# Optimization experiments

Measured on AMD Instinct MI355X. Metric: run time of the kernel, lower is better.

## Reference

```python
import jax, jax.numpy as jnp
import numpy as np

NUM_EXPERTS = 8
TOP_K = 2
CAPACITY_FACTOR = 1.25
D_MODEL = 2048
HIDDEN = 2048
N_TOKENS = 4096


def _expert_capacity(n_tokens):
    ideal = TOP_K * n_tokens / NUM_EXPERTS
    allowed = int(CAPACITY_FACTOR * ideal)
    return ((allowed + 7) // 8) * 8  # ensure_multiple_of(..., 8)


def setup_inputs() -> dict:
    key = jax.random.key(0)
    ks = jax.random.split(key, 6)
    x = jax.random.normal(ks[0], (N_TOKENS, D_MODEL), dtype=jnp.float32)
    ew = jax.random.uniform(ks[1], (N_TOKENS, TOP_K), dtype=jnp.float32)
    expert_weights = ew / jnp.sum(ew, axis=-1, keepdims=True)  # router softmax-like weights
    expert_indices = jax.random.randint(ks[2], (N_TOKENS, TOP_K), 0, NUM_EXPERTS, dtype=jnp.int32)
    s = 1.0 / np.sqrt(D_MODEL)
    w1 = jax.random.normal(ks[3], (NUM_EXPERTS, D_MODEL, HIDDEN), dtype=jnp.float32) * s
    w3 = jax.random.normal(ks[4], (NUM_EXPERTS, D_MODEL, HIDDEN), dtype=jnp.float32) * s
    w2 = jax.random.normal(ks[5], (NUM_EXPERTS, HIDDEN, D_MODEL), dtype=jnp.float32) * (1.0 / np.sqrt(HIDDEN))
    return {"x": x, "expert_weights": expert_weights, "expert_indices": expert_indices,
            "w1": w1, "w2": w2, "w3": w3}


def reference(x, expert_weights, expert_indices, w1, w2, w3):
    N, d = x.shape
    E = NUM_EXPERTS
    cap = _expert_capacity(N)
    T = N * TOP_K

    flat_e = expert_indices.reshape(-1)                      # [T]
    # histc: tokens per expert
    counts = jnp.zeros((E,), jnp.int32).at[flat_e].add(1)
    # stable sort by expert id (torch.sort on ints is stable here semantically)
    order = jnp.argsort(flat_e, stable=True)                 # [T]
    sorted_e = flat_e[order]
    starts = jnp.cumsum(counts) - counts                     # bin start offsets
    pos = jnp.arange(T, dtype=jnp.int32) - starts[sorted_e]  # rank within expert bin
    valid = pos < cap                                        # drop tokens over capacity
    tok = order // TOP_K                                     # source token per routed slot

    # binned_gather -> [E, cap, d]
    dest = jnp.where(valid, sorted_e * cap + pos, 0)
    xg = jnp.zeros((E * cap, d), x.dtype).at[dest].add(
        jnp.where(valid[:, None], x[tok], 0.0))
    xg = xg.reshape(E, cap, d)

    # grouped SwiGLU MLP per expert
    h = jax.nn.silu(jnp.einsum('ecd,edh->ech', xg, w1)) * jnp.einsum('ecd,edh->ech', xg, w3)
    ye = jnp.einsum('ech,ehd->ecd', h, w2).reshape(E * cap, d)

    # binned_scatter with expert weights (combine)
    w_flat = expert_weights.reshape(-1)[order]               # [T]
    contrib = ye[dest] * (w_flat * valid.astype(x.dtype))[:, None]
    y = jnp.zeros((N, d), x.dtype).at[tok].add(contrib)
    return y, counts
```

## Files before the change

### kernel.cpp

```cpp
#include <hip/hip_runtime.h>
#include <cstdint>

#define NEXP 8
#define TOPK 2
#define NTOK 4096
#define NSLOT (NTOK * TOPK)
#define CAP 1280
#define DM 2048
#define EC (NEXP * CAP)

typedef __bf16 bf16x8 __attribute__((ext_vector_type(8)));
typedef float  f32x4  __attribute__((ext_vector_type(4)));
typedef int    i32x4  __attribute__((ext_vector_type(4)));
typedef int    i32x8  __attribute__((ext_vector_type(8)));

typedef const void __attribute__((address_space(1))) gvoid;
typedef void __attribute__((address_space(3))) lvoid;

__device__ __forceinline__ void gld16(const void* g, void* l) {
  __builtin_amdgcn_global_load_lds((gvoid*)(uintptr_t)g, (lvoid*)(uintptr_t)l,
                                   16, 0, 0);
}

__device__ __forceinline__ unsigned fp8x4(float a, float b, float c, float d) {
  int v = __builtin_amdgcn_cvt_pk_fp8_f32(a, b, 0, false);
  v = __builtin_amdgcn_cvt_pk_fp8_f32(c, d, v, true);
  return (unsigned)v;
}
__device__ __forceinline__ unsigned char fp8one(float a) {
  return (unsigned char)(__builtin_amdgcn_cvt_pk_fp8_f32(a, a, 0, false) & 0xff);
}

__global__ void route_k(const int* __restrict__ eidx, int* __restrict__ row_token,
                        int* __restrict__ slot_dest, int* __restrict__ mcount,
                        float* __restrict__ out) {
  __shared__ int lh[256][NEXP];
  int tid = threadIdx.x;
  for (int i = tid; i < EC; i += 256) row_token[i] = -1;
#pragma unroll
  for (int e = 0; e < NEXP; ++e) lh[tid][e] = 0;
  __syncthreads();
  int base = tid * 32;
  for (int j = 0; j < 32; ++j) lh[tid][eidx[base + j]]++;
  __syncthreads();
  if (tid < NEXP) {
    int run = 0;
    for (int i = 0; i < 256; ++i) { int t = lh[i][tid]; lh[i][tid] = run; run += t; }
    mcount[tid] = run < CAP ? run : CAP;
    out[(size_t)NTOK * DM + tid] = (float)run;
  }
  __syncthreads();
  for (int j = 0; j < 32; ++j) {
    int t = base + j;
    int e = eidx[t];
    int r = lh[tid][e]++;
    if (r < CAP) { int dst = e * CAP + r; slot_dest[t] = dst; row_token[dst] = t >> 1; }
    else slot_dest[t] = -1;
  }
}

__device__ __forceinline__ void transT_tile(const float* __restrict__ w,
                                            unsigned char* __restrict__ wT,
                                            int e, int n0, int k0, char* smem) {
  float (*t)[69] = (float (*)[69])smem;
  const float* src = w + ((size_t)e << 22) + (size_t)k0 * DM + n0;
  unsigned char* dst = wT + ((size_t)e << 22) + (size_t)n0 * DM + k0;
  int c4 = (threadIdx.x & 15) * 4, r0 = threadIdx.x >> 4;
#pragma unroll
  for (int p = 0; p < 4; ++p) {
    int r = p * 16 + r0;
    float4 v = *(const float4*)(src + (size_t)r * DM + c4);
    t[r][c4 + 0] = v.x; t[r][c4 + 1] = v.y; t[r][c4 + 2] = v.z; t[r][c4 + 3] = v.w;
  }
  __syncthreads();
  int j = threadIdx.x & 7, rr0 = threadIdx.x >> 3;
#pragma unroll
  for (int q = 0; q < 2; ++q) {
    int rr = q * 32 + rr0;
    int k8 = j * 8;
    uint2 v;
    v.x = fp8x4(t[k8 + 0][rr], t[k8 + 1][rr], t[k8 + 2][rr], t[k8 + 3][rr]);
    v.y = fp8x4(t[k8 + 4][rr], t[k8 + 5][rr], t[k8 + 6][rr], t[k8 + 7][rr]);
    *(uint2*)(dst + (size_t)rr * DM + k8) = v;
  }
}

__global__ __launch_bounds__(256)
void prep_k(const float* __restrict__ w1, const float* __restrict__ w3,
            unsigned char* __restrict__ wT1, unsigned char* __restrict__ wT3,
            const float* __restrict__ x, const int* __restrict__ row_token,
            unsigned char* __restrict__ xg) {
  __shared__ __align__(16) char smem[64 * 69 * 4];
  int bid = blockIdx.x;
  if (bid < 16384) {
    const float* w = (bid & 8192) ? w3 : w1;
    unsigned char* wT = (bid & 8192) ? wT3 : wT1;
    int rem = bid & 8191;
    int e = rem >> 10, t = rem & 1023;
    transT_tile(w, wT, e, (t & 31) * 64, (t >> 5) * 64, smem);
  } else {
    int rbase = (bid - 16384) * 8;
    int c = threadIdx.x * 8;
#pragma unroll 1
    for (int i = 0; i < 8; ++i) {
      int r = rbase + i;
      int tok = row_token[r];
      uint2 o;
      if (tok >= 0) {
        const float* src = x + (size_t)tok * DM + c;
        float4 a = *(const float4*)src;
        float4 b = *(const float4*)(src + 4);
        o.x = fp8x4(a.x, a.y, a.z, a.w);
        o.y = fp8x4(b.x, b.y, b.z, b.w);
      } else { o.x = 0u; o.y = 0u; }
      *(uint2*)(xg + (size_t)r * DM + c) = o;
    }
  }
}

__global__ __launch_bounds__(256, 2)
void gemm13t_k(const unsigned char* __restrict__ A0, const unsigned char* __restrict__ B1T,
               const unsigned char* __restrict__ B3T, unsigned char* __restrict__ H,
               const int* __restrict__ mcount,
               const float* __restrict__ w2, unsigned char* __restrict__ wT2) {
  __shared__ __align__(16) char smem[48 * 1024];
  if (blockIdx.x >= 1280) {
    int rem = blockIdx.x - 1280;
    int e = rem >> 10, t = rem & 1023;
    transT_tile(w2, wT2, e, (t & 31) * 64, (t >> 5) * 64, smem);
    return;
  }
  int lbid = blockIdx.x;
  int nb = (lbid & 7) * 160 + (lbid >> 3);
  int e = nb / 160, rem = nb % 160, mt = rem >> 4, nt = rem & 15;
  int mc = mcount[e];
  if (mt * 128 >= mc) return;

  char* lA  = smem;
  char* lB1 = smem + 16384;
  char* lB3 = smem + 32768;

  int row0 = e * CAP + mt * 128;
  const unsigned char* gA  = A0 + (size_t)row0 * DM;
  size_t boff = ((size_t)e * DM + (size_t)nt * 128) * DM;
  const unsigned char* gB1 = B1T + boff;
  const unsigned char* gB3 = B3T + boff;

  int tid = threadIdx.x, w = tid >> 6, l = tid & 63;
  int wr = w >> 1, wc = w & 1;
  int lr = l & 15, kg = l >> 4;

  int sr = tid >> 3;
  int scs = (tid & 7) ^ (sr & 7);

  f32x4 acc1[4][4], acc3[4][4];
#pragma unroll
  for (int m = 0; m < 4; ++m)
#pragma unroll
    for (int n = 0; n < 4; ++n)
#pragma unroll
      for (int j = 0; j < 4; ++j) { acc1[m][n][j] = 0.f; acc3[m][n][j] = 0.f; }

  auto rdfrag = [&](const char* lX, int R) -> i32x8 {
    int r = R + lr;
    int a0 = r * 128 + (((2 * kg + 0) ^ (r & 7)) << 4);
    int a1 = r * 128 + (((2 * kg + 1) ^ (r & 7)) << 4);
    i32x4 lo = *(const i32x4*)(lX + a0);
    i32x4 hi = *(const i32x4*)(lX + a1);
    i32x8 v;
    v[0] = lo[0]; v[1] = lo[1]; v[2] = lo[2]; v[3] = lo[3];
    v[4] = hi[0]; v[5] = hi[1]; v[6] = hi[2]; v[7] = hi[3];
    return v;
  };

#pragma unroll 1
  for (int ks = 0; ks < 16; ++ks) {
#pragma unroll
    for (int s = 0; s < 4; ++s) {
      size_t goff = (size_t)(s * 32 + sr) * DM + (size_t)ks * 128 + scs * 16;
      gld16(gA  + goff, lA  + s * 4096 + w * 1024);
      gld16(gB1 + goff, lB1 + s * 4096 + w * 1024);
      gld16(gB3 + goff, lB3 + s * 4096 + w * 1024);
    }
    __syncthreads();
    i32x8 bf1[4], bf3[4];
#pragma unroll
    for (int n = 0; n < 4; ++n) bf1[n] = rdfrag(lB1, wc * 64 + n * 16);
#pragma unroll
    for (int n = 0; n < 4; ++n) bf3[n] = rdfrag(lB3, wc * 64 + n * 16);
#pragma unroll
    for (int m = 0; m < 4; ++m) {
      i32x8 af = rdfrag(lA, wr * 64 + m * 16);
#pragma unroll
      for (int n = 0; n < 4; ++n)
        acc1[m][n] = __builtin_amdgcn_mfma_scale_f32_16x16x128_f8f6f4(
            af, bf1[n], acc1[m][n], 0, 0, 0, 0x7F, 0, 0x7F);
#pragma unroll
      for (int n = 0; n < 4; ++n)
        acc3[m][n] = __builtin_amdgcn_mfma_scale_f32_16x16x128_f8f6f4(
            af, bf3[n], acc3[m][n], 0, 0, 0, 0x7F, 0, 0x7F);
    }
    __syncthreads();
  }

  int rg = l >> 4;
#pragma unroll
  for (int m = 0; m < 4; ++m)
#pragma unroll
    for (int n = 0; n < 4; ++n)
#pragma unroll
      for (int j = 0; j < 4; ++j) {
        int rr = row0 + wr * 64 + m * 16 + rg * 4 + j;
        int cc = nt * 128 + wc * 64 + n * 16 + lr;
        float u = acc1[m][n][j];
        float s = u / (1.f + __expf(-u));
        H[(size_t)rr * DM + cc] = fp8one(s * acc3[m][n][j]);
      }
}

__global__ __launch_bounds__(256, 4)
void gemm_k(const unsigned char* __restrict__ A0, const unsigned char* __restrict__ BT,
            __bf16* __restrict__ C, const int* __restrict__ mcount) {
  int lbid = blockIdx.x + 16 * (blockIdx.y + 10 * blockIdx.z);
  int nb = (lbid & 7) * 160 + (lbid >> 3);
  int e = nb / 160, rem = nb % 160, mt = rem >> 4, nt = rem & 15;
  int mc = mcount[e];
  if (mt * 128 >= mc) return;

  __shared__ __align__(16) char smem[32 * 1024];
  char* lA = smem;
  char* lB = smem + 16384;

  int row0 = e * CAP + mt * 128;
  const unsigned char* gA = A0 + (size_t)row0 * DM;
  const unsigned char* gB = BT + ((size_t)e * DM + (size_t)nt * 128) * DM;

  int tid = threadIdx.x, w = tid >> 6, l = tid & 63;
  int wr = w >> 1, wc = w & 1;
  int lr = l & 15, kg = l >> 4;

  int sr = tid >> 3;
  int scs = (tid & 7) ^ (sr & 7);

  f32x4 acc[4][4];
#pragma unroll
  for (int m = 0; m < 4; ++m)
#pragma unroll
    for (int n = 0; n < 4; ++n)
#pragma unroll
      for (int j = 0; j < 4; ++j) acc[m][n][j] = 0.f;

  auto rdfrag = [&](const char* lX, int R) -> i32x8 {
    int r = R + lr;
    int a0 = r * 128 + (((2 * kg + 0) ^ (r & 7)) << 4);
    int a1 = r * 128 + (((2 * kg + 1) ^ (r & 7)) << 4);
    i32x4 lo = *(const i32x4*)(lX + a0);
    i32x4 hi = *(const i32x4*)(lX + a1);
    i32x8 v;
    v[0] = lo[0]; v[1] = lo[1]; v[2] = lo[2]; v[3] = lo[3];
    v[4] = hi[0]; v[5] = hi[1]; v[6] = hi[2]; v[7] = hi[3];
    return v;
  };

#pragma unroll 1
  for (int ks = 0; ks < 16; ++ks) {
#pragma unroll
    for (int s = 0; s < 4; ++s) {
      size_t goff = (size_t)(s * 32 + sr) * DM + (size_t)ks * 128 + scs * 16;
      gld16(gA + goff, lA + s * 4096 + w * 1024);
      gld16(gB + goff, lB + s * 4096 + w * 1024);
    }
    __syncthreads();
    i32x8 bf[4];
#pragma unroll
    for (int n = 0; n < 4; ++n) bf[n] = rdfrag(lB, wc * 64 + n * 16);
#pragma unroll
    for (int m = 0; m < 4; ++m) {
      i32x8 af = rdfrag(lA, wr * 64 + m * 16);
#pragma unroll
      for (int n = 0; n < 4; ++n)
        acc[m][n] = __builtin_amdgcn_mfma_scale_f32_16x16x128_f8f6f4(
            af, bf[n], acc[m][n], 0, 0, 0, 0x7F, 0, 0x7F);
    }
    __syncthreads();
  }

  int rg = l >> 4;
#pragma unroll
  for (int m = 0; m < 4; ++m)
#pragma unroll
    for (int n = 0; n < 4; ++n)
#pragma unroll
      for (int j = 0; j < 4; ++j) {
        int rr = row0 + wr * 64 + m * 16 + rg * 4 + j;
        int cc = nt * 128 + wc * 64 + n * 16 + lr;
        C[(size_t)rr * DM + cc] = (__bf16)acc[m][n][j];
      }
}

__global__ void combine_k(const __bf16* __restrict__ ye, const int* __restrict__ slot_dest,
                          const float* __restrict__ ew, float* __restrict__ out) {
  int tok = blockIdx.x;
  int c = threadIdx.x * 8;
  int d0 = slot_dest[2 * tok], d1 = slot_dest[2 * tok + 1];
  float w0 = ew[2 * tok], w1 = ew[2 * tok + 1];
  float r[8];
#pragma unroll
  for (int j = 0; j < 8; ++j) r[j] = 0.f;
  if (d0 >= 0) {
    bf16x8 y0 = *(const bf16x8*)(ye + (size_t)d0 * DM + c);
#pragma unroll
    for (int j = 0; j < 8; ++j) r[j] += w0 * (float)y0[j];
  }
  if (d1 >= 0) {
    bf16x8 y1 = *(const bf16x8*)(ye + (size_t)d1 * DM + c);
#pragma unroll
    for (int j = 0; j < 8; ++j) r[j] += w1 * (float)y1[j];
  }
  float* dst = out + (size_t)tok * DM + c;
  float4 o0; o0.x = r[0]; o0.y = r[1]; o0.z = r[2]; o0.w = r[3];
  float4 o1; o1.x = r[4]; o1.y = r[5]; o1.z = r[6]; o1.w = r[7];
  *(float4*)dst = o0;
  *(float4*)(dst + 4) = o1;
}

extern "C" void kernel_launch(void* const* d_in, const int* in_sizes, int n_in,
                              void* d_out, int out_size, void* d_ws, size_t ws_size,
                              hipStream_t stream) {
  const float* x  = (const float*)d_in[0];
  const float* ew = (const float*)d_in[1];
  const int*   ei = (const int*)d_in[2];
  const float* w1 = (const float*)d_in[3];
  const float* w2 = (const float*)d_in[4];
  const float* w3 = (const float*)d_in[5];
  float* out = (float*)d_out;
  char* ws = (char*)d_ws;

  const size_t SZ8  = (size_t)EC * DM;
  const size_t SZ16 = 2 * SZ8;
  const size_t SZW  = (size_t)NEXP * DM * DM;
  unsigned char* xg  = (unsigned char*)ws;
  __bf16* yeB        = (__bf16*)(ws + SZ8);
  unsigned char* hB  = (unsigned char*)(ws + SZ8 + SZ16);
  unsigned char* wT1 = (unsigned char*)(ws + 2 * SZ8 + SZ16);
  unsigned char* wT3 = (unsigned char*)(ws + 2 * SZ8 + SZ16 + SZW);
  unsigned char* wT2 = (unsigned char*)(ws + 2 * SZ8 + SZ16 + 2 * SZW);
  char* ints = ws + 2 * SZ8 + SZ16 + 3 * SZW;
  int* row_token = (int*)ints;
  int* slot_dest = row_token + EC;
  int* mcount    = slot_dest + NSLOT;

  dim3 ggrid(16, 10, NEXP);

  route_k<<<1, 256, 0, stream>>>(ei, row_token, slot_dest, mcount, out);
  prep_k<<<17664, 256, 0, stream>>>(w1, w3, wT1, wT3, x, row_token, xg);
  gemm13t_k<<<9472, 256, 0, stream>>>(xg, wT1, wT3, hB, mcount, w2, wT2);
  gemm_k<<<ggrid, 256, 0, stream>>>(hB, wT2, yeB, mcount);
  combine_k<<<NTOK, 256, 0, stream>>>(yeB, slot_dest, ew, out);
}
```

Baseline: 265.6 us.

## Quantize expert weights to FP4 and use mixed FP8xFP4 scaled MFMA

Weights are now transposed and quantized to packed FP4 (e2m1) with a fixed ×64 prescale, halving weight bytes written in prep and read in both GEMMs. B tiles are loaded every other k-step and fed to the scaled MFMA with FP4 format for B, and the accumulators are rescaled by 1/64 in the epilogues. This reduces weight memory traffic and transpose-write bandwidth at a large cost in numerical accuracy, since a single global scale with FP4 may exceed the tolerance.

```diff
diff --git a/kernel.cpp b/kernel.cpp
--- a/kernel.cpp
+++ b/kernel.cpp
@@ -8,6 +8,8 @@
 #define CAP 1280
 #define DM 2048
 #define EC (NEXP * CAP)
+#define KB4 1024
+#define INV64 0.015625f
 
 typedef __bf16 bf16x8 __attribute__((ext_vector_type(8)));
 typedef float  f32x4  __attribute__((ext_vector_type(4)));
@@ -29,6 +31,15 @@
 }
 __device__ __forceinline__ unsigned char fp8one(float a) {
   return (unsigned char)(__builtin_amdgcn_cvt_pk_fp8_f32(a, a, 0, false) & 0xff);
+}
+
+__device__ __forceinline__ unsigned qfp4(float x) {
+  float a = fabsf(x);
+  unsigned s = (__float_as_uint(x) >> 28) & 8u;
+  unsigned r = (a < 0.25f) ? 0u : (a < 0.75f) ? 1u : (a < 1.25f) ? 2u
+             : (a < 1.75f) ? 3u : (a < 2.5f)  ? 4u : (a < 3.5f)  ? 5u
+             : (a < 5.0f)  ? 6u : 7u;
+  return s | r;
 }
 
 __global__ void route_k(const int* __restrict__ eidx, int* __restrict__ row_token,
@@ -60,11 +71,11 @@
 }
 
 __device__ __forceinline__ void transT_tile(const float* __restrict__ w,
-                                            unsigned char* __restrict__ wT,
+                                            unsigned char* __restrict__ wT4,
                                             int e, int n0, int k0, char* smem) {
   float (*t)[69] = (float (*)[69])smem;
   const float* src = w + ((size_t)e << 22) + (size_t)k0 * DM + n0;
-  unsigned char* dst = wT + ((size_t)e << 22) + (size_t)n0 * DM + k0;
+  unsigned char* dst = wT4 + ((size_t)e * DM + n0) * KB4 + (k0 >> 1);
   int c4 = (threadIdx.x & 15) * 4, r0 = threadIdx.x >> 4;
 #pragma unroll
   for (int p = 0; p < 4; ++p) {
@@ -77,11 +88,11 @@
 #pragma unroll
   for (int q = 0; q < 2; ++q) {
     int rr = q * 32 + rr0;
-    int k8 = j * 8;
-    uint2 v;
-    v.x = fp8x4(t[k8 + 0][rr], t[k8 + 1][rr], t[k8 + 2][rr], t[k8 + 3][rr]);
-    v.y = fp8x4(t[k8 + 4][rr], t[k8 + 5][rr], t[k8 + 6][rr], t[k8 + 7][rr]);
-    *(uint2*)(dst + (size_t)rr * DM + k8) = v;
+    unsigned p = 0;
+#pragma unroll
+    for (int i = 0; i < 8; ++i)
+      p |= qfp4(t[j * 8 + i][rr] * 64.f) << (4 * i);
+    *(unsigned*)(dst + (size_t)rr * KB4 + j * 4) = p;
   }
 }
 
@@ -142,7 +153,7 @@
 
   int row0 = e * CAP + mt * 128;
   const unsigned char* gA  = A0 + (size_t)row0 * DM;
-  size_t boff = ((size_t)e * DM + (size_t)nt * 128) * DM;
+  size_t boff = ((size_t)e * DM + (size_t)nt * 128) * KB4;
   const unsigned char* gB1 = B1T + boff;
   const unsigned char* gB3 = B3T + boff;
 
@@ -161,44 +172,61 @@
 #pragma unroll
       for (int j = 0; j < 4; ++j) { acc1[m][n][j] = 0.f; acc3[m][n][j] = 0.f; }
 
-  auto rdfrag = [&](const char* lX, int R) -> i32x8 {
+  auto rdA = [&](int R) -> i32x8 {
     int r = R + lr;
-    int a0 = r * 128 + (((2 * kg + 0) ^ (r & 7)) << 4);
-    int a1 = r * 128 + (((2 * kg + 1) ^ (r & 7)) << 4);
-    i32x4 lo = *(const i32x4*)(lX + a0);
-    i32x4 hi = *(const i32x4*)(lX + a1);
+    i32x4 lo = *(const i32x4*)(lA + r * 128 + (((2 * kg + 0) ^ (r & 7)) << 4));
+    i32x4 hi = *(const i32x4*)(lA + r * 128 + (((2 * kg + 1) ^ (r & 7)) << 4));
     i32x8 v;
     v[0] = lo[0]; v[1] = lo[1]; v[2] = lo[2]; v[3] = lo[3];
     v[4] = hi[0]; v[5] = hi[1]; v[6] = hi[2]; v[7] = hi[3];
     return v;
   };
+  auto rdB4 = [&](const char* lX, int R, int half) -> i32x4 {
+    int r = R + lr;
+    int c = half * 4 + kg;
+    return *(const i32x4*)(lX + r * 128 + ((c ^ (r & 7)) << 4));
+  };
+  auto mk8 = [](i32x4 d) -> i32x8 {
+    i32x8 v;
+    v[0] = d[0]; v[1] = d[1]; v[2] = d[2]; v[3] = d[3];
+    v[4] = 0; v[5] = 0; v[6] = 0; v[7] = 0;
+    return v;
+  };
 
 #pragma unroll 1
   for (int ks = 0; ks < 16; ++ks) {
 #pragma unroll
     for (int s = 0; s < 4; ++s) {
-      size_t goff = (size_t)(s * 32 + sr) * DM + (size_t)ks * 128 + scs * 16;
-      gld16(gA  + goff, lA  + s * 4096 + w * 1024);
-      gld16(gB1 + goff, lB1 + s * 4096 + w * 1024);
-      gld16(gB3 + goff, lB3 + s * 4096 + w * 1024);
+      gld16(gA + (size_t)(s * 32 + sr) * DM + (size_t)ks * 128 + scs * 16,
+            lA + s * 4096 + w * 1024);
+    }
+    if ((ks & 1) == 0) {
+      size_t t4 = (size_t)(ks >> 1) * 128;
+#pragma unroll
+      for (int s = 0; s < 4; ++s) {
+        size_t goff = (size_t)(s * 32 + sr) * KB4 + t4 + scs * 16;
+        gld16(gB1 + goff, lB1 + s * 4096 + w * 1024);
+        gld16(gB3 + goff, lB3 + s * 4096 + w * 1024);
+      }
     }
     __syncthreads();
-    i32x8 bf1[4], bf3[4];
-#pragma unroll
-    for (int n = 0; n < 4; ++n) bf1[n] = rdfrag(lB1, wc * 64 + n * 16);
-#pragma unroll
-    for (int n = 0; n < 4; ++n) bf3[n] = rdfrag(lB3, wc * 64 + n * 16);
+    int half = ks & 1;
+    i32x4 bf1[4], bf3[4];
+#pragma unroll
+    for (int n = 0; n < 4; ++n) bf1[n] = rdB4(lB1, wc * 64 + n * 16, half);
+#pragma unroll
+    for (int n = 0; n < 4; ++n) bf3[n] = rdB4(lB3, wc * 64 + n * 16, half);
 #pragma unroll
     for (int m = 0; m < 4; ++m) {
-      i32x8 af = rdfrag(lA, wr * 64 + m * 16);
+      i32x8 af = rdA(wr * 64 + m * 16);
 #pragma unroll
       for (int n = 0; n < 4; ++n)
         acc1[m][n] = __builtin_amdgcn_mfma_scale_f32_16x16x128_f8f6f4(
-            af, bf1[n], acc1[m][n], 0, 0, 0, 0x7F, 0, 0x7F);
+            af, mk8(bf1[n]), acc1[m][n], 0, 4, 0, 0x7F, 0, 0x7F);
 #pragma unroll
       for (int n = 0; n < 4; ++n)
         acc3[m][n] = __builtin_amdgcn_mfma_scale_f32_16x16x128_f8f6f4(
-            af, bf3[n], acc3[m][n], 0, 0, 0, 0x7F, 0, 0x7F);
+            af, mk8(bf3[n]), acc3[m][n], 0, 4, 0, 0x7F, 0, 0x7F);
     }
     __syncthreads();
   }
@@ -212,9 +240,10 @@
       for (int j = 0; j < 4; ++j) {
         int rr = row0 + wr * 64 + m * 16 + rg * 4 + j;
         int cc = nt * 128 + wc * 64 + n * 16 + lr;
-        float u = acc1[m][n][j];
+        float u = acc1[m][n][j] * INV64;
+        float v = acc3[m][n][j] * INV64;
         float s = u / (1.f + __expf(-u));
-        H[(size_t)rr * DM + cc] = fp8one(s * acc3[m][n][j]);
+        H[(size_t)rr * DM + cc] = fp8one(s * v);
       }
 }
 
@@ -233,7 +262,7 @@
 
   int row0 = e * CAP + mt * 128;
   const unsigned char* gA = A0 + (size_t)row0 * DM;
-  const unsigned char* gB = BT + ((size_t)e * DM + (size_t)nt * 128) * DM;
+  const unsigned char* gB = BT + ((size_t)e * DM + (size_t)nt * 128) * KB4;
 
   int tid = threadIdx.x, w = tid >> 6, l = tid & 63;
   int wr = w >> 1, wc = w & 1;
@@ -250,37 +279,53 @@
 #pragma unroll
       for (int j = 0; j < 4; ++j) acc[m][n][j] = 0.f;
 
-  auto rdfrag = [&](const char* lX, int R) -> i32x8 {
+  auto rdA = [&](int R) -> i32x8 {
     int r = R + lr;
-    int a0 = r * 128 + (((2 * kg + 0) ^ (r & 7)) << 4);
-    int a1 = r * 128 + (((2 * kg + 1) ^ (r & 7)) << 4);
-    i32x4 lo = *(const i32x4*)(lX + a0);
-    i32x4 hi = *(const i32x4*)(lX + a1);
+    i32x4 lo = *(const i32x4*)(lA + r * 128 + (((2 * kg + 0) ^ (r & 7)) << 4));
+    i32x4 hi = *(const i32x4*)(lA + r * 128 + (((2 * kg + 1) ^ (r & 7)) << 4));
     i32x8 v;
     v[0] = lo[0]; v[1] = lo[1]; v[2] = lo[2]; v[3] = lo[3];
     v[4] = hi[0]; v[5] = hi[1]; v[6] = hi[2]; v[7] = hi[3];
     return v;
   };
+  auto rdB4 = [&](int R, int half) -> i32x4 {
+    int r = R + lr;
+    int c = half * 4 + kg;
+    return *(const i32x4*)(lB + r * 128 + ((c ^ (r & 7)) << 4));
+  };
+  auto mk8 = [](i32x4 d) -> i32x8 {
+    i32x8 v;
+    v[0] = d[0]; v[1] = d[1]; v[2] = d[2]; v[3] = d[3];
+    v[4] = 0; v[5] = 0; v[6] = 0; v[7] = 0;
+    return v;
+  };
 
 #pragma unroll 1
   for (int ks = 0; ks < 16; ++ks) {
 #pragma unroll
     for (int s = 0; s < 4; ++s) {
-      size_t goff = (size_t)(s * 32 + sr) * DM + (size_t)ks * 128 + scs * 16;
-      gld16(gA + goff, lA + s * 4096 + w * 1024);
-      gld16(gB + goff, lB + s * 4096 + w * 1024);
+      gld16(gA + (size_t)(s * 32 + sr) * DM + (size_t)ks * 128 + scs * 16,
+            lA + s * 4096 + w * 1024);
+    }
+    if ((ks & 1) == 0) {
+      size_t t4 = (size_t)(ks >> 1) * 128;
+#pragma unroll
+      for (int s = 0; s < 4; ++s)
+        gld16(gB + (size_t)(s * 32 + sr) * KB4 + t4 + scs * 16,
+              lB + s * 4096 + w * 1024);
     }
     __syncthreads();
-    i32x8 bf[4];
-#pragma unroll
-    for (int n = 0; n < 4; ++n) bf[n] = rdfrag(lB, wc * 64 + n * 16);
+    int half = ks & 1;
+    i32x4 bf[4];
+#pragma unroll
+    for (int n = 0; n < 4; ++n) bf[n] = rdB4(wc * 64 + n * 16, half);
 #pragma unroll
     for (int m = 0; m < 4; ++m) {
-      i32x8 af = rdfrag(lA, wr * 64 + m * 16);
+      i32x8 af = rdA(wr * 64 + m * 16);
 #pragma unroll
       for (int n = 0; n < 4; ++n)
         acc[m][n] = __builtin_amdgcn_mfma_scale_f32_16x16x128_f8f6f4(
-            af, bf[n], acc[m][n], 0, 0, 0, 0x7F, 0, 0x7F);
+            af, mk8(bf[n]), acc[m][n], 0, 4, 0, 0x7F, 0, 0x7F);
     }
     __syncthreads();
   }
@@ -294,7 +339,7 @@
       for (int j = 0; j < 4; ++j) {
         int rr = row0 + wr * 64 + m * 16 + rg * 4 + j;
         int cc = nt * 128 + wc * 64 + n * 16 + lr;
-        C[(size_t)rr * DM + cc] = (__bf16)acc[m][n][j];
+        C[(size_t)rr * DM + cc] = (__bf16)(acc[m][n][j] * INV64);
       }
 }
 
@@ -338,14 +383,14 @@
 
   const size_t SZ8  = (size_t)EC * DM;
   const size_t SZ16 = 2 * SZ8;
-  const size_t SZW  = (size_t)NEXP * DM * DM;
+  const size_t SZW4 = (size_t)NEXP * DM * KB4;
   unsigned char* xg  = (unsigned char*)ws;
   __bf16* yeB        = (__bf16*)(ws + SZ8);
   unsigned char* hB  = (unsigned char*)(ws + SZ8 + SZ16);
   unsigned char* wT1 = (unsigned char*)(ws + 2 * SZ8 + SZ16);
-  unsigned char* wT3 = (unsigned char*)(ws + 2 * SZ8 + SZ16 + SZW);
-  unsigned char* wT2 = (unsigned char*)(ws + 2 * SZ8 + SZ16 + 2 * SZW);
-  char* ints = ws + 2 * SZ8 + SZ16 + 3 * SZW;
+  unsigned char* wT3 = (unsigned char*)(ws + 2 * SZ8 + SZ16 + SZW4);
+  unsigned char* wT2 = (unsigned char*)(ws + 2 * SZ8 + SZ16 + 2 * SZW4);
+  char* ints = ws + 2 * SZ8 + SZ16 + 3 * SZW4;
   int* row_token = (int*)ints;
   int* slot_dest = row_token + EC;
   int* mcount    = slot_dest + NSLOT;
```

Measured after the change: 267.1 us. About the same (+0.6%).
